# Optimization experiments

Hardware: AMD Instinct MI355X
Metric: run time of the kernel (lower is better)

Reference implementation:

```python
import jax, jax.numpy as jnp
import numpy as np

TS = 16      # tile size
ST = 4       # stride
IN = 224     # image size
G = (IN - TS) // ST + 1   # 53 tiles per side
L = G * G                 # 2809 tiles
CH = [3 * L, 3 * L // 4, 3 * L // 16, 3 * L // 4, 3 * L]  # [8427,2106,526,2106,8427]

# torch_dct-style unnormalized DCT-II matrix and its exact inverse (DCT-III based)
_n = np.arange(TS)
_k = np.arange(TS)[:, None]
_C = np.cos(np.pi * (2 * _n[None, :] + 1) * _k / (2 * TS))  # [k, n]
D_DCT = jnp.asarray(2.0 * _C, jnp.float32)                   # dct: y = D @ x
_w = np.ones(TS); _w[0] = 0.5
D_IDCT = jnp.asarray((_C.T * _w[None, :]) / TS, jnp.float32) # idct: x = Dinv @ y

# gather/scatter indices for unfold/fold (constants)
IH = (np.arange(G) * ST)[:, None] + np.arange(TS)[None, :]   # [G, TS]
IW = IH


def setup_inputs() -> dict:
    key = jax.random.key(0)
    ks = jax.random.split(key, 9)
    x = jax.random.normal(ks[0], (8, 3, IN, IN), jnp.float32)
    def lin(k, o, c):
        return jax.random.normal(k, (o, c), jnp.float32) * 0.02
    return {
        'x': x,
        'w1': lin(ks[1], CH[1], CH[0]), 'b1': jnp.zeros((CH[1],), jnp.float32),
        'w2': lin(ks[2], CH[2], CH[1]), 'b2': jnp.zeros((CH[2],), jnp.float32),
        'w3': lin(ks[3], CH[3], CH[2]), 'b3': jnp.zeros((CH[3],), jnp.float32),
        'w4': lin(ks[4], CH[4], CH[3]), 'b4': jnp.zeros((CH[4],), jnp.float32),
    }


def _forward(x, w1, b1, w2, b2, w3, b3, w4, b4):
    b = x.shape[0]
    # unfold: gather overlapping 16x16 patches -> [b, 3, G, G, TS, TS]
    p = x[:, :, IH[:, None, :, None], IW[None, :, None, :]]
    # torch ordering after permute+reshape: channel index = l*3 + c
    tiles = p.transpose(0, 2, 3, 1, 4, 5).reshape(b, 3 * L, TS, TS)
    # 2D DCT (unnormalized DCT-II along last two dims)
    dct_tiles = jnp.einsum('km,ln,bcmn->bckl', D_DCT, D_DCT, tiles)
    # mask net: stack of 1x1 convs over the tile-channel dim
    h = dct_tiles / (TS * TS)
    h = jax.nn.relu(jnp.einsum('oc,bchw->bohw', w1, h) + b1[:, None, None])
    h = jax.nn.relu(jnp.einsum('oc,bchw->bohw', w2, h) + b2[:, None, None])
    h = jax.nn.relu(jnp.einsum('oc,bchw->bohw', w3, h) + b3[:, None, None])
    masks = jax.nn.sigmoid(jnp.einsum('oc,bchw->bohw', w4, h) + b4[:, None, None])
    clean_dct = masks * dct_tiles
    # 2D inverse DCT
    clean_tiles = jnp.einsum('mk,nl,bckl->bcmn', D_IDCT, D_IDCT, clean_dct)
    # fold: scatter-add patches back with overlap
    ct = clean_tiles.reshape(b, G, G, 3, TS, TS).transpose(0, 3, 1, 2, 4, 5)
    out = jnp.zeros((b, 3, IN, IN), x.dtype)
    out = out.at[:, :, IH[:, None, :, None], IW[None, :, None, :]].add(ct)
    # scale = fold(unfold(ones)): per-pixel overlap counts (recomputed per call, as in source)
    scale = jnp.zeros((IN, IN), x.dtype)
    scale = scale.at[IH[:, None, :, None], IW[None, :, None, :]].add(
        jnp.ones((G, G, TS, TS), x.dtype))
    return out / scale


def reference(x, w1, b1, w2, b2, w3, b3, w4, b4):
    return _forward(x, w1, b1, w2, b2, w3, b3, w4, b4)
```

## Files before the change

### kernel.cpp

```cpp
#include <hip/hip_runtime.h>
#include <stdint.h>

constexpr int INSZ = 224;
constexpr int GD   = 53;
constexpr int C0R = 8427, C1R = 2106, C2R = 526;
constexpr int C0P = 8448, C1P = 2176, C2P = 640;
constexpr int NTOK = 2048;

typedef __attribute__((ext_vector_type(4))) float f32x4;
typedef __attribute__((ext_vector_type(8))) short bf16x8;

constexpr float CT[64] = {
  1.00000000f,  0.99518473f,  0.98078528f,  0.95694034f,
  0.92387953f,  0.88192126f,  0.83146961f,  0.77301045f,
  0.70710678f,  0.63439328f,  0.55557023f,  0.47139674f,
  0.38268343f,  0.29028468f,  0.19509032f,  0.09801714f,
  0.00000000f, -0.09801714f, -0.19509032f, -0.29028468f,
 -0.38268343f, -0.47139674f, -0.55557023f, -0.63439328f,
 -0.70710678f, -0.77301045f, -0.83146961f, -0.88192126f,
 -0.92387953f, -0.95694034f, -0.98078528f, -0.99518473f,
 -1.00000000f, -0.99518473f, -0.98078528f, -0.95694034f,
 -0.92387953f, -0.88192126f, -0.83146961f, -0.77301045f,
 -0.70710678f, -0.63439328f, -0.55557023f, -0.47139674f,
 -0.38268343f, -0.29028468f, -0.19509032f, -0.09801714f,
 -0.00000000f,  0.09801714f,  0.19509032f,  0.29028468f,
  0.38268343f,  0.47139674f,  0.55557023f,  0.63439328f,
  0.70710678f,  0.77301045f,  0.83146961f,  0.88192126f,
  0.92387953f,  0.95694034f,  0.98078528f,  0.99518473f
};
constexpr float Dfwd(int k, int n) { return 2.0f * CT[((2 * n + 1) * k) & 63]; }
constexpr float Dinv(int n, int k) { return CT[((2 * n + 1) * k) & 63] * (k == 0 ? 0.03125f : 0.0625f); }

constexpr int TRS_R = 20, TRS_T = 336;
constexpr int TRS_SZ = 15 * TRS_T + 15 * TRS_R + 16;

__device__ __forceinline__ unsigned short f2bf(float f) {
  union { float f; unsigned u; } v; v.f = f;
  return (unsigned short)((v.u + 0x7FFFu + ((v.u >> 16) & 1u)) >> 16);
}
__device__ __forceinline__ float bf2f(unsigned short b) {
  union { unsigned u; float f; } v; v.u = ((unsigned)b) << 16;
  return v.f;
}

__device__ __forceinline__ void gload_lds16(const void* g, void* l) {
  __builtin_amdgcn_global_load_lds(
      (__attribute__((address_space(1))) unsigned int*)(uintptr_t)g,
      (__attribute__((address_space(3))) unsigned int*)(unsigned int)(uintptr_t)l,
      16, 0, 0);
}

__device__ __forceinline__ void xcd_tile(int& bx, int& by) {
  const int gx = gridDim.x, gy = gridDim.y;
  const int nwg = gx * gy;
  const int bid = blockIdx.y * gx + blockIdx.x;
  const int cpx = nwg >> 3;
  const int l = (bid & 7) * cpx + (bid >> 3);
  const int stripe = gy << 2;
  const int bxg = l / stripe;
  const int r = l - bxg * stripe;
  const int rem = gx - (bxg << 2);
  const int w = rem < 4 ? rem : 4;
  by = r / w;
  bx = (bxg << 2) + (r - by * w);
}

__global__ void cvt_pad(const float* __restrict__ src, unsigned short* __restrict__ dst,
                        int M, int K, int Kp) {
  const int k = blockIdx.x * 256 + threadIdx.x;
  const int m = blockIdx.y;
  if (k >= Kp) return;
  const float v = (m < M && k < K) ? src[(size_t)m * K + k] : 0.f;
  dst[(size_t)m * Kp + k] = f2bf(v);
}

constexpr int CVA1 = C2P * C1P;
constexpr int CVA2 = CVA1 + C1P * C2P;
constexpr int CVTOT = CVA2 + C0P * C1P;
__global__ void cvt_pad_all(const float* __restrict__ w2, const float* __restrict__ w3,
                            const float* __restrict__ w4, unsigned short* __restrict__ d2,
                            unsigned short* __restrict__ d3, unsigned short* __restrict__ d4) {
  const int i = blockIdx.x * 256 + threadIdx.x;
  if (i < CVA1) {
    const int m = i / C1P, k = i - m * C1P;
    d2[i] = f2bf((m < C2R && k < C1R) ? w2[(size_t)m * C1R + k] : 0.f);
  } else if (i < CVA2) {
    const int j = i - CVA1;
    const int m = j / C2P, k = j - m * C2P;
    d3[j] = f2bf((m < C1R && k < C2R) ? w3[(size_t)m * C2R + k] : 0.f);
  } else {
    const int j = i - CVA2;
    const int m = j / C1P, k = j - m * C1P;
    d4[j] = f2bf((m < C0R && k < C1R) ? w4[(size_t)m * C1R + k] : 0.f);
  }
}

__global__ __launch_bounds__(256)
void dct_h0(const float* __restrict__ x, unsigned short* __restrict__ H0) {
  __shared__ float trp[TRS_SZ];
  __shared__ unsigned short hst[256 * 64];
  const int tid = threadIdx.x;
  const int b   = blockIdx.y;
  const int c0  = blockIdx.x * 64;
  const int t = tid >> 4, q = tid & 15;

  for (int g = 0; g < 4; ++g) {
    const int c = c0 + g * 16 + t;
    float p[16];
    {
      float4 v0{}, v1{}, v2{}, v3{};
      if (c < C0R) {
        const int ch = c % 3, gw = (c / 3) % GD, gh = c / (3 * GD);
        const float* xr = x + ((size_t)(b * 3 + ch) * INSZ + (gh * 4 + q)) * INSZ + gw * 4;
        v0 = *(const float4*)(xr);      v1 = *(const float4*)(xr + 4);
        v2 = *(const float4*)(xr + 8);  v3 = *(const float4*)(xr + 12);
      }
      p[0]=v0.x; p[1]=v0.y; p[2]=v0.z; p[3]=v0.w;
      p[4]=v1.x; p[5]=v1.y; p[6]=v1.z; p[7]=v1.w;
      p[8]=v2.x; p[9]=v2.y; p[10]=v2.z; p[11]=v2.w;
      p[12]=v3.x; p[13]=v3.y; p[14]=v3.z; p[15]=v3.w;
    }
    float r[16];
#pragma unroll
    for (int k = 0; k < 16; ++k) {
      float s = 0.f;
#pragma unroll
      for (int n = 0; n < 16; ++n) s += p[n] * Dfwd(k, n);
      r[k] = s;
    }
    float* wr = &trp[t * TRS_T + q * TRS_R];
#pragma unroll
    for (int k = 0; k < 16; k += 4)
      *(float4*)(wr + k) = make_float4(r[k], r[k+1], r[k+2], r[k+3]);
    __syncthreads();
    const int j = q;
    float rr[16];
#pragma unroll
    for (int i = 0; i < 16; ++i) rr[i] = trp[t * TRS_T + i * TRS_R + j];
#pragma unroll
    for (int k = 0; k < 16; ++k) {
      float s = 0.f;
#pragma unroll
      for (int i = 0; i < 16; ++i) s += rr[i] * Dfwd(k, i);
      hst[(k * 16 + j) * 64 + g * 16 + t] = f2bf(s * (1.f / 256.f));
    }
    __syncthreads();
  }
  const size_t base = ((size_t)b * 256) * C0P + c0;
#pragma unroll
  for (int i = 0; i < 8; ++i) {
    const int s = i * 256 + tid;
    const int kl = s >> 3, c16 = s & 7;
    *(uint4*)&H0[base + (size_t)kl * C0P + c16 * 8] = *(const uint4*)&hst[kl * 64 + c16 * 8];
  }
}

template<int OUT_NM>
__device__ __forceinline__ void gemm_core(
    const unsigned short* __restrict__ W, const unsigned short* __restrict__ Ht,
    unsigned short (*As)[128 * 32], unsigned short (*Bs)[128 * 32],
    int m0, int n0, int Kp, int kbase, int nkt, int w, int lane, f32x4 acc[4][4]) {
  const int wr = w >> 1, wc = w & 1;
  const int lhi = lane >> 4, llo = lane & 15;

  const int chunk0 = w * 64 + lane;
  const int row0 = chunk0 >> 2, kc0 = chunk0 & 3;
  const int kcg0 = kc0 ^ ((row0 >> 1) & 3);
  const int chunk1 = 256 + w * 64 + lane;
  const int row1 = chunk1 >> 2, kc1 = chunk1 & 3;
  const int kcg1 = kc1 ^ ((row1 >> 1) & 3);

  auto STAGE = [&](int kt, int sel) {
    const int kb = kbase + kt * 32;
    gload_lds16(W  + (size_t)(m0 + row0) * Kp + kb + kcg0 * 8, &As[sel][(w * 64) * 8]);
    gload_lds16(Ht + (size_t)(n0 + row0) * Kp + kb + kcg0 * 8, &Bs[sel][(w * 64) * 8]);
    gload_lds16(W  + (size_t)(m0 + row1) * Kp + kb + kcg1 * 8, &As[sel][(256 + w * 64) * 8]);
    gload_lds16(Ht + (size_t)(n0 + row1) * Kp + kb + kcg1 * 8, &Bs[sel][(256 + w * 64) * 8]);
  };

  STAGE(0, 0);
  if (nkt > 1) STAGE(1, 1);

  int cur = 0, nxt = 1, nx2 = 2;
  for (int kt = 0; kt < nkt; ++kt) {
    if (kt + 1 < nkt) {
      asm volatile("s_waitcnt vmcnt(4)" ::: "memory");
      __builtin_amdgcn_s_barrier();
      __builtin_amdgcn_sched_barrier(0);
      if (kt + 2 < nkt) STAGE(kt + 2, nx2);
    } else {
      asm volatile("s_waitcnt vmcnt(0)" ::: "memory");
      __builtin_amdgcn_s_barrier();
      __builtin_amdgcn_sched_barrier(0);
    }
    bf16x8 af[4], bfr[4];
#pragma unroll
    for (int mi = 0; mi < 4; ++mi) {
      const int row = wr * 64 + mi * 16 + llo;
      af[mi] = *(const bf16x8*)(&As[cur][row * 32 + (lhi ^ ((row >> 1) & 3)) * 8]);
    }
#pragma unroll
    for (int ni = 0; ni < 4; ++ni) {
      const int row = wc * 64 + ni * 16 + llo;
      bfr[ni] = *(const bf16x8*)(&Bs[cur][row * 32 + (lhi ^ ((row >> 1) & 3)) * 8]);
    }
#pragma unroll
    for (int mi = 0; mi < 4; ++mi)
#pragma unroll
      for (int ni = 0; ni < 4; ++ni) {
        if (OUT_NM)
          acc[mi][ni] = __builtin_amdgcn_mfma_f32_16x16x32_bf16(bfr[ni], af[mi], acc[mi][ni], 0, 0, 0);
        else
          acc[mi][ni] = __builtin_amdgcn_mfma_f32_16x16x32_bf16(af[mi], bfr[ni], acc[mi][ni], 0, 0, 0);
      }
    const int tmp = cur; cur = nxt; nxt = nx2; nx2 = tmp;
  }
}

template<int ACT, int OUT_NM>
__global__ __launch_bounds__(256)
void gemm_bt(const unsigned short* __restrict__ W, const unsigned short* __restrict__ Ht,
             const float* __restrict__ bias, int Mreal,
             unsigned short* __restrict__ out, int ldo, int Kp) {
  __shared__ unsigned short As[3][128 * 32];
  __shared__ unsigned short Bs[3][128 * 32];
  int bx, by; xcd_tile(bx, by);
  const int tid = threadIdx.x;
  const int w = tid >> 6, lane = tid & 63;
  const int m0 = bx * 128, n0 = by * 128;
  const int wr = w >> 1, wc = w & 1;
  const int lhi = lane >> 4, llo = lane & 15;

  f32x4 acc[4][4];
#pragma unroll
  for (int i = 0; i < 4; ++i)
#pragma unroll
    for (int j = 0; j < 4; ++j) acc[i][j] = f32x4{0.f, 0.f, 0.f, 0.f};

  gemm_core<OUT_NM>(W, Ht, As, Bs, m0, n0, Kp, 0, Kp >> 5, w, lane, acc);

  if (OUT_NM) {
#pragma unroll
    for (int mi = 0; mi < 4; ++mi) {
      const int mg = m0 + wr * 64 + mi * 16 + llo;
      const float bv = (mg < Mreal) ? bias[mg] : 0.f;
#pragma unroll
      for (int ni = 0; ni < 4; ++ni) {
        const int ng = n0 + wc * 64 + ni * 16 + lhi * 4;
#pragma unroll
        for (int r = 0; r < 4; ++r) {
          float v = acc[mi][ni][r] + bv;
          if (ACT == 1) v = fmaxf(v, 0.f);
          else if (ACT == 2) v = 1.f / (1.f + expf(-v));
          out[(size_t)(ng + r) * ldo + mg] = f2bf(v);
        }
      }
    }
  } else {
#pragma unroll
    for (int mi = 0; mi < 4; ++mi) {
      const int mgb = m0 + wr * 64 + mi * 16 + lhi * 4;
#pragma unroll
      for (int ni = 0; ni < 4; ++ni) {
        const int ng = n0 + wc * 64 + ni * 16 + llo;
#pragma unroll
        for (int r = 0; r < 4; ++r) {
          const int mg = mgb + r;
          float v = acc[mi][ni][r] + ((mg < Mreal) ? bias[mg] : 0.f);
          if (ACT == 1) v = fmaxf(v, 0.f);
          else if (ACT == 2) v = 1.f / (1.f + expf(-v));
          out[(size_t)mg * ldo + ng] = f2bf(v);
        }
      }
    }
  }
}

__global__ __launch_bounds__(256)
void gemm_splitk(const unsigned short* __restrict__ W, const unsigned short* __restrict__ Ht,
                 float* __restrict__ part, int ldo , int Kp, int chunkK) {
  __shared__ unsigned short As[3][128 * 32];
  __shared__ unsigned short Bs[3][128 * 32];
  int bx, by; xcd_tile(bx, by);
  const int z = blockIdx.z;
  const int tid = threadIdx.x;
  const int w = tid >> 6, lane = tid & 63;
  const int m0 = bx * 128, n0 = by * 128;
  const int wr = w >> 1, wc = w & 1;
  const int lhi = lane >> 4, llo = lane & 15;

  f32x4 acc[4][4];
#pragma unroll
  for (int i = 0; i < 4; ++i)
#pragma unroll
    for (int j = 0; j < 4; ++j) acc[i][j] = f32x4{0.f, 0.f, 0.f, 0.f};

  gemm_core<1>(W, Ht, As, Bs, m0, n0, Kp, z * chunkK, chunkK >> 5, w, lane, acc);

  float* pz = part + (size_t)z * NTOK * ldo;
#pragma unroll
  for (int mi = 0; mi < 4; ++mi) {
    const int mg = m0 + wr * 64 + mi * 16 + llo;
#pragma unroll
    for (int ni = 0; ni < 4; ++ni) {
      const int ng = n0 + wc * 64 + ni * 16 + lhi * 4;
#pragma unroll
      for (int r = 0; r < 4; ++r)
        pz[(size_t)(ng + r) * ldo + mg] = acc[mi][ni][r];
    }
  }
}

__global__ __launch_bounds__(256)
void reduce_act(const float* __restrict__ part, const float* __restrict__ bias,
                unsigned short* __restrict__ out, int Mp, int Mreal, int nch) {
  const int i4 = blockIdx.x * 256 + threadIdx.x;
  const int total = NTOK * Mp / 4;
  if (i4 >= total) return;
  const size_t off = (size_t)i4 * 4;
  const int m0 = (int)(off % Mp);
  float s0 = 0.f, s1 = 0.f, s2 = 0.f, s3 = 0.f;
  for (int z = 0; z < nch; ++z) {
    const float4 v = *(const float4*)(part + (size_t)z * NTOK * Mp + off);
    s0 += v.x; s1 += v.y; s2 += v.z; s3 += v.w;
  }
  s0 += (m0 + 0 < Mreal) ? bias[m0 + 0] : 0.f;
  s1 += (m0 + 1 < Mreal) ? bias[m0 + 1] : 0.f;
  s2 += (m0 + 2 < Mreal) ? bias[m0 + 2] : 0.f;
  s3 += (m0 + 3 < Mreal) ? bias[m0 + 3] : 0.f;
  s0 = fmaxf(s0, 0.f); s1 = fmaxf(s1, 0.f); s2 = fmaxf(s2, 0.f); s3 = fmaxf(s3, 0.f);
  uint2 pk;
  pk.x = (unsigned)f2bf(s0) | ((unsigned)f2bf(s1) << 16);
  pk.y = (unsigned)f2bf(s2) | ((unsigned)f2bf(s3) << 16);
  *(uint2*)&out[off] = pk;
}

__global__ __launch_bounds__(256)
void mask_idct(const float* __restrict__ x, const unsigned short* __restrict__ masks,
               unsigned short* __restrict__ clean) {
  __shared__ float trp[TRS_SZ];
  const int tid = threadIdx.x;
  const int b   = blockIdx.y;
  const int c0  = blockIdx.x * 16;
  const int t = tid >> 4, q = tid & 15;
  const int c = c0 + t;
  const bool valid = (c < C0R);

  float p[16];
  {
    float4 v0{}, v1{}, v2{}, v3{};
    if (valid) {
      const int ch = c % 3, gw = (c / 3) % GD, gh = c / (3 * GD);
      const float* xr = x + ((size_t)(b * 3 + ch) * INSZ + (gh * 4 + q)) * INSZ + gw * 4;
      v0 = *(const float4*)(xr);      v1 = *(const float4*)(xr + 4);
      v2 = *(const float4*)(xr + 8);  v3 = *(const float4*)(xr + 12);
    }
    p[0]=v0.x; p[1]=v0.y; p[2]=v0.z; p[3]=v0.w;
    p[4]=v1.x; p[5]=v1.y; p[6]=v1.z; p[7]=v1.w;
    p[8]=v2.x; p[9]=v2.y; p[10]=v2.z; p[11]=v2.w;
    p[12]=v3.x; p[13]=v3.y; p[14]=v3.z; p[15]=v3.w;
  }
  float r[16];
#pragma unroll
  for (int k = 0; k < 16; ++k) {
    float s = 0.f;
#pragma unroll
    for (int n = 0; n < 16; ++n) s += p[n] * Dfwd(k, n);
    r[k] = s;
  }
  {
    float* wr = &trp[t * TRS_T + q * TRS_R];
#pragma unroll
    for (int k = 0; k < 16; k += 4)
      *(float4*)(wr + k) = make_float4(r[k], r[k+1], r[k+2], r[k+3]);
  }
  __syncthreads();
  const int j = q;
  float rr[16];
#pragma unroll
  for (int i = 0; i < 16; ++i) rr[i] = trp[t * TRS_T + i * TRS_R + j];
  float cd[16];
  const unsigned short* mrow = masks + (size_t)c * NTOK + (size_t)b * 256 + j;
#pragma unroll
  for (int k = 0; k < 16; ++k) {
    float s = 0.f;
#pragma unroll
    for (int i = 0; i < 16; ++i) s += rr[i] * Dfwd(k, i);
    const float mv = valid ? bf2f(mrow[k * 16]) : 0.f;
    cd[k] = s * mv;
  }
  float t3[16];
#pragma unroll
  for (int m = 0; m < 16; ++m) {
    float s = 0.f;
#pragma unroll
    for (int k = 0; k < 16; ++k) s += cd[k] * Dinv(m, k);
    t3[m] = s;
  }
  __syncthreads();
  {
    float* wr = &trp[t * TRS_T + j * TRS_R];
#pragma unroll
    for (int m = 0; m < 16; m += 4)
      *(float4*)(wr + m) = make_float4(t3[m], t3[m+1], t3[m+2], t3[m+3]);
  }
  __syncthreads();
  float tr[16];
#pragma unroll
  for (int l = 0; l < 16; ++l) tr[l] = trp[t * TRS_T + l * TRS_R + q];
  if (valid) {
    unsigned pk[8];
#pragma unroll
    for (int n2 = 0; n2 < 8; ++n2) {
      float s0 = 0.f, s1 = 0.f;
#pragma unroll
      for (int l = 0; l < 16; ++l) {
        s0 += tr[l] * Dinv(2 * n2, l);
        s1 += tr[l] * Dinv(2 * n2 + 1, l);
      }
      pk[n2] = (unsigned)f2bf(s0) | ((unsigned)f2bf(s1) << 16);
    }
    unsigned short* dst = clean + ((size_t)b * C0R + c) * 256 + q * 16;
    uint4* d4 = (uint4*)dst;
    d4[0] = make_uint4(pk[0], pk[1], pk[2], pk[3]);
    d4[1] = make_uint4(pk[4], pk[5], pk[6], pk[7]);
  }
}

__global__ void overlap_add(const unsigned short* __restrict__ clean, float* __restrict__ out) {
  const int px = blockIdx.x * 256 + threadIdx.x;
  if (px >= 8 * 3 * 224 * 224) return;
  const int j = px % 224;
  const int i = (px / 224) % 224;
  const int bc = px / (224 * 224);
  const int ch = bc % 3, b = bc / 3;
  const int ilo = i - 15;
  const int ghlo = ilo > 0 ? (ilo + 3) >> 2 : 0;
  const int ghhi = (i >> 2) < 52 ? (i >> 2) : 52;
  const int jlo = j - 15;
  const int gwlo = jlo > 0 ? (jlo + 3) >> 2 : 0;
  const int gwhi = (j >> 2) < 52 ? (j >> 2) : 52;
  float sum = 0.f;
  for (int gh = ghlo; gh <= ghhi; ++gh) {
    const int r = i - gh * 4;
    const size_t base = ((size_t)b * C0R + (size_t)gh * (3 * GD) + ch) * 256 + (size_t)r * 16 + j;
    for (int gw = gwlo; gw <= gwhi; ++gw) {
      sum += bf2f(clean[base + (size_t)gw * 764]);
    }
  }
  const int cnt = (ghhi - ghlo + 1) * (gwhi - gwlo + 1);
  out[px] = sum / (float)cnt;
}

extern "C" void kernel_launch(void* const* d_in, const int* in_sizes, int n_in,
                              void* d_out, int out_size, void* d_ws, size_t ws_size,
                              hipStream_t stream) {
  const float* x  = (const float*)d_in[0];
  const float* w1 = (const float*)d_in[1];
  const float* b1 = (const float*)d_in[2];
  const float* w2 = (const float*)d_in[3];
  const float* b2 = (const float*)d_in[4];
  const float* w3 = (const float*)d_in[5];
  const float* b3 = (const float*)d_in[6];
  const float* w4 = (const float*)d_in[7];
  const float* b4 = (const float*)d_in[8];
  float* out = (float*)d_out;
  char* ws = (char*)d_ws;

  const size_t S_WB1  = (size_t)C1P * C0P * 2;
  const size_t S_H0   = (size_t)NTOK * C0P * 2;
  const size_t S_PART = (size_t)3 * NTOK * C1P * 4;
  const size_t OFF_WB1  = 0;
  const size_t OFF_H0   = OFF_WB1 + S_WB1;
  const size_t OFF_PART = OFF_H0 + S_H0;
  const size_t OFF_Y1   = OFF_PART + S_PART;

  unsigned short* wb1 = (unsigned short*)(ws + OFF_WB1);
  unsigned short* H0v = (unsigned short*)(ws + OFF_H0);
  float*          pt1 = (float*)(ws + OFF_PART);
  unsigned short* Y1  = (unsigned short*)(ws + OFF_Y1);
  unsigned short* wb2 = (unsigned short*)(ws + OFF_PART);
  unsigned short* wb3 = (unsigned short*)(ws + OFF_PART + (size_t)C2P * C1P * 2);
  unsigned short* wb4 = (unsigned short*)(ws + OFF_PART + (size_t)2 * C2P * C1P * 2);
  unsigned short* Y2  = (unsigned short*)(ws + OFF_PART + (size_t)2 * C2P * C1P * 2 + (size_t)C0P * C1P * 2);
  float*          pt2 = (float*)(ws + OFF_WB1);
  float*          pt3 = (float*)(ws + OFF_WB1);
  unsigned short* clean = (unsigned short*)(ws + OFF_WB1);
  unsigned short* Y3  = (unsigned short*)(ws + OFF_Y1);
  unsigned short* msk = (unsigned short*)(ws + OFF_H0);

  cvt_pad<<<dim3((C0P + 255) / 256, C1P), 256, 0, stream>>>(w1, wb1, C1R, C0R, C0P);
  dct_h0<<<dim3(C0P / 64, 8), 256, 0, stream>>>(x, H0v);

  gemm_splitk<<<dim3(C1P / 128, NTOK / 128, 3), 256, 0, stream>>>(wb1, H0v, pt1, C1P, C0P, 2816);
  reduce_act<<<dim3(NTOK * C1P / 4 / 256), 256, 0, stream>>>(pt1, b1, Y1, C1P, C1R, 3);

  cvt_pad_all<<<dim3(CVTOT / 256), 256, 0, stream>>>(w2, w3, w4, wb2, wb3, wb4);

  gemm_splitk<<<dim3(C2P / 128, NTOK / 128, 4), 256, 0, stream>>>(wb2, Y1, pt2, C2P, C1P, 544);
  reduce_act<<<dim3(NTOK * C2P / 4 / 256), 256, 0, stream>>>(pt2, b2, Y2, C2P, C2R, 4);

  gemm_splitk<<<dim3(C1P / 128, NTOK / 128, 2), 256, 0, stream>>>(wb3, Y2, pt3, C1P, C2P, 320);
  reduce_act<<<dim3(NTOK * C1P / 4 / 256), 256, 0, stream>>>(pt3, b3, Y3, C1P, C1R, 2);

  gemm_bt<2, 0><<<dim3(C0P / 128, NTOK / 128), 256, 0, stream>>>(wb4, Y3, b4, C0R, msk, NTOK, C1P);

  mask_idct<<<dim3((C0R + 15) / 16, 8), 256, 0, stream>>>(x, msk, clean);

  overlap_add<<<dim3((8 * 3 * 224 * 224 + 255) / 256), 256, 0, stream>>>(clean, out);
}
```

Before: 466.5 us.

## Add 256x256-tile triple-buffered GEMM for the two large layers

Adds a 512-thread GEMM kernel with 256x256 output tiles, three-stage LDS buffering and split A/B staging interleaved with MFMA halves. It is used for the first split-K layer and for most of the final sigmoid layer, with the old kernel handling the remaining rows. C1P is padded to 2304 so it divides by 256, and the workspace offsets are laid out again to match. The goal is more operand reuse per load on the two biggest GEMMs. The cost is extra padded K/N work, heavier register and LDS use per block, and fewer blocks in flight.

Measured after the change: 434.4 us. 6.9% less time.

```diff
diff --git a/kernel.cpp b/kernel.cpp
--- a/kernel.cpp
+++ b/kernel.cpp
@@ -4,7 +4,7 @@
 constexpr int INSZ = 224;
 constexpr int GD   = 53;
 constexpr int C0R = 8427, C1R = 2106, C2R = 526;
-constexpr int C0P = 8448, C1P = 2176, C2P = 640;
+constexpr int C0P = 8448, C1P = 2304, C2P = 640;
 constexpr int NTOK = 2048;
 
 typedef __attribute__((ext_vector_type(4))) float f32x4;
@@ -155,6 +155,132 @@
   }
 }
 
+template<int ACT, int OUT_NM, int SPLITK>
+__global__ __launch_bounds__(512, 2)
+void gemm256(const unsigned short* __restrict__ W, const unsigned short* __restrict__ Ht,
+             const float* __restrict__ bias, void* __restrict__ outp,
+             int ldo, int Kp, int chunkK) {
+  __shared__ unsigned short As[3][8192];
+  __shared__ unsigned short Bs[3][8192];
+  int bx, by; xcd_tile(bx, by);
+  const int m0 = bx * 256, n0 = by * 256;
+  const int tid = threadIdx.x;
+  const int w = tid >> 6, lane = tid & 63;
+  const int wr = w >> 2, wc = w & 3;
+  const int lhi = lane >> 4, llo = lane & 15;
+  const int kbase = SPLITK ? blockIdx.z * chunkK : 0;
+  const int nkt = chunkK >> 5;
+
+  const int srow = tid >> 2;
+  const int slgc = ((tid & 3) ^ ((srow >> 1) & 3)) * 8;
+
+  f32x4 acc[8][4];
+#pragma unroll
+  for (int i = 0; i < 8; ++i)
+#pragma unroll
+    for (int j = 0; j < 4; ++j) acc[i][j] = f32x4{0.f, 0.f, 0.f, 0.f};
+
+  auto STAGE_A = [&](int kt, int buf) {
+    const int kb = kbase + kt * 32 + slgc;
+    gload_lds16(W + (size_t)(m0 + srow) * Kp + kb,       &As[buf][w * 512]);
+    gload_lds16(W + (size_t)(m0 + 128 + srow) * Kp + kb, &As[buf][4096 + w * 512]);
+  };
+  auto STAGE_B = [&](int kt, int buf) {
+    const int kb = kbase + kt * 32 + slgc;
+    gload_lds16(Ht + (size_t)(n0 + srow) * Kp + kb,       &Bs[buf][w * 512]);
+    gload_lds16(Ht + (size_t)(n0 + 128 + srow) * Kp + kb, &Bs[buf][4096 + w * 512]);
+  };
+
+  STAGE_A(0, 0); STAGE_B(0, 0);
+  if (nkt > 1) { STAGE_A(1, 1); STAGE_B(1, 1); }
+
+  int buf = 0;
+  for (int kt = 0; kt < nkt; ++kt) {
+    const int sbuf = buf >= 1 ? buf - 1 : 2;
+    if (kt + 1 < nkt) asm volatile("s_waitcnt vmcnt(4)" ::: "memory");
+    else              asm volatile("s_waitcnt vmcnt(0)" ::: "memory");
+    __builtin_amdgcn_s_barrier();
+    __builtin_amdgcn_sched_barrier(0);
+
+    bf16x8 af[4], bfr[4];
+#pragma unroll
+    for (int mi = 0; mi < 4; ++mi) {
+      const int row = wr * 128 + mi * 16 + llo;
+      af[mi] = *(const bf16x8*)(&As[buf][row * 32 + ((lhi ^ ((row >> 1) & 3)) << 3)]);
+    }
+#pragma unroll
+    for (int ni = 0; ni < 4; ++ni) {
+      const int row = wc * 64 + ni * 16 + llo;
+      bfr[ni] = *(const bf16x8*)(&Bs[buf][row * 32 + ((lhi ^ ((row >> 1) & 3)) << 3)]);
+    }
+    if (kt + 2 < nkt) STAGE_A(kt + 2, sbuf);
+    __builtin_amdgcn_s_setprio(1);
+#pragma unroll
+    for (int mi = 0; mi < 4; ++mi)
+#pragma unroll
+      for (int ni = 0; ni < 4; ++ni)
+        acc[mi][ni] = OUT_NM
+          ? __builtin_amdgcn_mfma_f32_16x16x32_bf16(bfr[ni], af[mi], acc[mi][ni], 0, 0, 0)
+          : __builtin_amdgcn_mfma_f32_16x16x32_bf16(af[mi], bfr[ni], acc[mi][ni], 0, 0, 0);
+    __builtin_amdgcn_s_setprio(0);
+    __builtin_amdgcn_s_barrier();
+    __builtin_amdgcn_sched_barrier(0);
+#pragma unroll
+    for (int mi = 0; mi < 4; ++mi) {
+      const int row = wr * 128 + 64 + mi * 16 + llo;
+      af[mi] = *(const bf16x8*)(&As[buf][row * 32 + ((lhi ^ ((row >> 1) & 3)) << 3)]);
+    }
+    if (kt + 2 < nkt) STAGE_B(kt + 2, sbuf);
+    __builtin_amdgcn_s_setprio(1);
+#pragma unroll
+    for (int mi = 0; mi < 4; ++mi)
+#pragma unroll
+      for (int ni = 0; ni < 4; ++ni)
+        acc[4 + mi][ni] = OUT_NM
+          ? __builtin_amdgcn_mfma_f32_16x16x32_bf16(bfr[ni], af[mi], acc[4 + mi][ni], 0, 0, 0)
+          : __builtin_amdgcn_mfma_f32_16x16x32_bf16(af[mi], bfr[ni], acc[4 + mi][ni], 0, 0, 0);
+    __builtin_amdgcn_s_setprio(0);
+    buf = buf == 2 ? 0 : buf + 1;
+  }
+
+  if (SPLITK) {
+    float* pz = (float*)outp + (size_t)blockIdx.z * ((size_t)NTOK * ldo);
+#pragma unroll
+    for (int mh = 0; mh < 2; ++mh)
+#pragma unroll
+      for (int mi = 0; mi < 4; ++mi) {
+        const int mg = m0 + wr * 128 + mh * 64 + mi * 16 + llo;
+#pragma unroll
+        for (int ni = 0; ni < 4; ++ni) {
+          const int ng = n0 + wc * 64 + ni * 16 + lhi * 4;
+#pragma unroll
+          for (int r = 0; r < 4; ++r)
+            pz[(size_t)(ng + r) * ldo + mg] = acc[mh * 4 + mi][ni][r];
+        }
+      }
+  } else {
+    unsigned short* out = (unsigned short*)outp;
+#pragma unroll
+    for (int mh = 0; mh < 2; ++mh)
+#pragma unroll
+      for (int mi = 0; mi < 4; ++mi) {
+        const int mgb = m0 + wr * 128 + mh * 64 + mi * 16 + lhi * 4;
+#pragma unroll
+        for (int ni = 0; ni < 4; ++ni) {
+          const int ng = n0 + wc * 64 + ni * 16 + llo;
+#pragma unroll
+          for (int r = 0; r < 4; ++r) {
+            const int mg = mgb + r;
+            float v = acc[mh * 4 + mi][ni][r] + bias[mg];
+            if (ACT == 1) v = fmaxf(v, 0.f);
+            else if (ACT == 2) v = 1.f / (1.f + expf(-v));
+            out[(size_t)mg * ldo + ng] = f2bf(v);
+          }
+        }
+      }
+  }
+}
+
 template<int OUT_NM>
 __device__ __forceinline__ void gemm_core(
     const unsigned short* __restrict__ W, const unsigned short* __restrict__ Ht,
@@ -467,43 +593,46 @@
   float* out = (float*)d_out;
   char* ws = (char*)d_ws;
 
-  const size_t S_WB1  = (size_t)C1P * C0P * 2;
-  const size_t S_H0   = (size_t)NTOK * C0P * 2;
-  const size_t S_PART = (size_t)3 * NTOK * C1P * 4;
-  const size_t OFF_WB1  = 0;
-  const size_t OFF_H0   = OFF_WB1 + S_WB1;
-  const size_t OFF_PART = OFF_H0 + S_H0;
-  const size_t OFF_Y1   = OFF_PART + S_PART;
-
-  unsigned short* wb1 = (unsigned short*)(ws + OFF_WB1);
-  unsigned short* H0v = (unsigned short*)(ws + OFF_H0);
-  float*          pt1 = (float*)(ws + OFF_PART);
-  unsigned short* Y1  = (unsigned short*)(ws + OFF_Y1);
-  unsigned short* wb2 = (unsigned short*)(ws + OFF_PART);
-  unsigned short* wb3 = (unsigned short*)(ws + OFF_PART + (size_t)C2P * C1P * 2);
-  unsigned short* wb4 = (unsigned short*)(ws + OFF_PART + (size_t)2 * C2P * C1P * 2);
-  unsigned short* Y2  = (unsigned short*)(ws + OFF_PART + (size_t)2 * C2P * C1P * 2 + (size_t)C0P * C1P * 2);
-  float*          pt2 = (float*)(ws + OFF_WB1);
-  float*          pt3 = (float*)(ws + OFF_WB1);
-  unsigned short* clean = (unsigned short*)(ws + OFF_WB1);
-  unsigned short* Y3  = (unsigned short*)(ws + OFF_Y1);
-  unsigned short* msk = (unsigned short*)(ws + OFF_H0);
+  const size_t OFF_A = 0;
+  const size_t OFF_B = 38928384;
+  const size_t OFF_C = 73531392;
+
+  unsigned short* wb1   = (unsigned short*)(ws + OFF_A);
+  unsigned short* wb4   = (unsigned short*)(ws + OFF_A);
+  unsigned short* clean = (unsigned short*)(ws + OFF_A);
+
+  unsigned short* H0v = (unsigned short*)(ws + OFF_B);
+  unsigned short* Y1  = (unsigned short*)(ws + OFF_B);
+  unsigned short* wb2 = (unsigned short*)(ws + OFF_B + 9437184);
+  unsigned short* wb3 = (unsigned short*)(ws + OFF_B + 12386304);
+  unsigned short* Y2  = (unsigned short*)(ws + OFF_B + 15335424);
+  unsigned short* msk = (unsigned short*)(ws + OFF_B);
+
+  float* pt1 = (float*)(ws + OFF_C);
+  float* pt2 = (float*)(ws + OFF_C);
+  float* pt3 = (float*)(ws + OFF_C);
+  unsigned short* Y3 = (unsigned short*)(ws + OFF_C + 37748736);
 
   cvt_pad<<<dim3((C0P + 255) / 256, C1P), 256, 0, stream>>>(w1, wb1, C1R, C0R, C0P);
   dct_h0<<<dim3(C0P / 64, 8), 256, 0, stream>>>(x, H0v);
 
-  gemm_splitk<<<dim3(C1P / 128, NTOK / 128, 3), 256, 0, stream>>>(wb1, H0v, pt1, C1P, C0P, 2816);
+  gemm256<0, 1, 1><<<dim3(C1P / 256, NTOK / 256, 3), 512, 0, stream>>>(
+      wb1, H0v, nullptr, pt1, C1P, C0P, 2816);
   reduce_act<<<dim3(NTOK * C1P / 4 / 256), 256, 0, stream>>>(pt1, b1, Y1, C1P, C1R, 3);
 
   cvt_pad_all<<<dim3(CVTOT / 256), 256, 0, stream>>>(w2, w3, w4, wb2, wb3, wb4);
 
-  gemm_splitk<<<dim3(C2P / 128, NTOK / 128, 4), 256, 0, stream>>>(wb2, Y1, pt2, C2P, C1P, 544);
+  gemm_splitk<<<dim3(C2P / 128, NTOK / 128, 4), 256, 0, stream>>>(wb2, Y1, pt2, C2P, C1P, 576);
   reduce_act<<<dim3(NTOK * C2P / 4 / 256), 256, 0, stream>>>(pt2, b2, Y2, C2P, C2R, 4);
 
   gemm_splitk<<<dim3(C1P / 128, NTOK / 128, 2), 256, 0, stream>>>(wb3, Y2, pt3, C1P, C2P, 320);
   reduce_act<<<dim3(NTOK * C1P / 4 / 256), 256, 0, stream>>>(pt3, b3, Y3, C1P, C1R, 2);
 
-  gemm_bt<2, 0><<<dim3(C0P / 128, NTOK / 128), 256, 0, stream>>>(wb4, Y3, b4, C0R, msk, NTOK, C1P);
+  gemm256<2, 0, 0><<<dim3(32, NTOK / 256), 512, 0, stream>>>(
+      wb4, Y3, b4, msk, NTOK, C1P, C1P);
+  gemm_bt<2, 0><<<dim3(2, NTOK / 128), 256, 0, stream>>>(
+      wb4 + (size_t)8192 * C1P, Y3, b4 + 8192, C0R - 8192,
+      msk + (size_t)8192 * NTOK, NTOK, C1P);
 
   mask_idct<<<dim3((C0R + 15) / 16, 8), 256, 0, stream>>>(x, msk, clean);
 
```
